# Kernel optimization log

Hardware: AMD Instinct MI355X
Metric: run time of the kernel (lower is better)

## Reference

```python
import jax, jax.numpy as jnp
import numpy as np

N_NODES = 100000
N_EDGES = 3200000
ENTITY_DIM = 128
LAYER_DIMS = [128, 64, 32]


def setup_inputs() -> dict:
    key = jax.random.key(0)
    ks = jax.random.split(key, 20)
    inp = {
        "x": jax.random.normal(ks[0], (N_NODES, ENTITY_DIM), dtype=jnp.float32) * 0.1,
        "src_idx": jax.random.randint(ks[1], (N_EDGES,), 0, N_NODES, dtype=jnp.int32),
        "dst_idx": jax.random.randint(ks[2], (N_EDGES,), 0, N_NODES, dtype=jnp.int32),
        "edge_attn": jax.random.uniform(ks[3], (N_EDGES,), dtype=jnp.float32),
    }
    in_dim = ENTITY_DIM
    ki = 4
    for li, out_dim in enumerate(LAYER_DIMS):
        scale = jnp.sqrt(2.0 / (in_dim + out_dim)).astype(jnp.float32)
        inp[f"W1_{li}"] = jax.random.normal(ks[ki], (in_dim, out_dim), dtype=jnp.float32) * scale
        inp[f"b1_{li}"] = jnp.zeros((out_dim,), dtype=jnp.float32)
        inp[f"W2_{li}"] = jax.random.normal(ks[ki + 1], (in_dim, out_dim), dtype=jnp.float32) * scale
        inp[f"b2_{li}"] = jnp.zeros((out_dim,), dtype=jnp.float32)
        ki += 2
        in_dim = out_dim
    return inp


def _kgat_layer(x, src_idx, dst_idx, a, W1, b1, W2, b2):
    # edge-weighted sparse aggregation: h_n[v] = sum_{(u->v)} a_e * x[u]
    msgs = x[src_idx] * a[:, None]                       # [E, D] gather + scale
    h_n = jax.ops.segment_sum(msgs, dst_idx, num_segments=x.shape[0])  # [N, D]
    # bi-interaction fuse
    out = jax.nn.leaky_relu((x + h_n) @ W1 + b1) + jax.nn.leaky_relu((x * h_n) @ W2 + b2)
    return out


def reference(x, src_idx, dst_idx, edge_attn,
              W1_0, b1_0, W2_0, b2_0,
              W1_1, b1_1, W2_1, b2_1,
              W1_2, b1_2, W2_2, b2_2):
    params = [(W1_0, b1_0, W2_0, b2_0), (W1_1, b1_1, W2_1, b2_1), (W1_2, b1_2, W2_2, b2_2)]
    embs = [x]
    h = x
    for (W1, b1, W2, b2) in params:
        h = _kgat_layer(h, src_idx, dst_idx, edge_attn, W1, b1, W2, b2)
        embs.append(h)
    return jnp.concatenate(embs, axis=1)  # [N, 128+128+64+32]
```

## Files before the change

kernel.cpp:

```cpp
#include <hip/hip_runtime.h>
#include <hip/hip_bf16.h>

#define LRELU_SLOPE 0.01f

typedef __attribute__((ext_vector_type(8))) short short8;
typedef __attribute__((ext_vector_type(4))) float f32x4;

__device__ __forceinline__ unsigned int f2bf_rne(float f) {
    unsigned int u = __float_as_uint(f);
    u += 0x7FFFu + ((u >> 16) & 1u);
    return u >> 16;
}
__device__ __forceinline__ float bf_lo(unsigned int u) { return __uint_as_float(u << 16); }
__device__ __forceinline__ float bf_hi(unsigned int u) { return __uint_as_float(u & 0xFFFF0000u); }

__global__ void bucket_count_kernel(const int* __restrict__ dst,
                                    int* __restrict__ bucket_total, int E, int NB) {
    __shared__ int cnt[512];
    const int t = threadIdx.x;
    const int tile0 = blockIdx.x * 8192;
    for (int i = t; i < 512; i += 256) cnt[i] = 0;
    __syncthreads();
#pragma unroll
    for (int j = 0; j < 32; ++j) {
        int e = tile0 + j * 256 + t;
        if (e < E) atomicAdd(&cnt[dst[e] >> 8], 1);
    }
    __syncthreads();
    for (int i = t; i < NB; i += 256) {
        int c = cnt[i];
        if (c) atomicAdd(&bucket_total[i], c);
    }
}

__global__ void bucket_scan_kernel(const int* __restrict__ bucket_total,
                                   int* __restrict__ bucket_base,
                                   int* __restrict__ row_ptr, int NB, int n) {
    __shared__ int s[512];
    const int t = threadIdx.x;
    int c = (t < NB) ? bucket_total[t] : 0;
    s[t] = c;
    __syncthreads();
    for (int off = 1; off < 512; off <<= 1) {
        int v = (t >= off) ? s[t - off] : 0;
        __syncthreads();
        s[t] += v;
        __syncthreads();
    }
    if (t < NB) bucket_base[t] = s[t] - c;
    if (t == 511) {
        bucket_base[NB] = s[511];
        row_ptr[n] = s[511];
    }
}

__global__ void bucket_scatter_kernel(const int* __restrict__ dst,
                                      const int* __restrict__ src,
                                      const float* __restrict__ attn,
                                      const int* __restrict__ bucket_base,
                                      int* __restrict__ bucket_fill,
                                      int2* __restrict__ bsa,
                                      int E, int NB) {
    __shared__ int cnt[512];
    __shared__ int basef[512];
    const int t = threadIdx.x;
    const int tile0 = blockIdx.x * 4096;
    for (int i = t; i < 512; i += 256) cnt[i] = 0;
    __syncthreads();
    int d[16], lr[16];
#pragma unroll
    for (int j = 0; j < 16; ++j) {
        int e = tile0 + j * 256 + t;
        if (e < E) {
            d[j] = dst[e];
            lr[j] = atomicAdd(&cnt[d[j] >> 8], 1);
        }
    }
    __syncthreads();
    for (int i = t; i < NB; i += 256) {
        int c = cnt[i];
        int r = c ? atomicAdd(&bucket_fill[i], c) : 0;
        basef[i] = bucket_base[i] + r;
    }
    __syncthreads();
#pragma unroll
    for (int j = 0; j < 16; ++j) {
        int e = tile0 + j * 256 + t;
        if (e < E) {
            int pos = basef[d[j] >> 8] + lr[j];
            unsigned int px = ((unsigned int)src[e] << 8) | (unsigned int)(d[j] & 255);
            bsa[pos] = make_int2((int)px, __float_as_int(attn[e]));
        }
    }
}

__global__ void bucket_build_kernel(const int* __restrict__ bucket_base,
                                    const int2* __restrict__ bsa,
                                    int* __restrict__ row_ptr, int2* __restrict__ csr_edge,
                                    int n) {
    __shared__ int cnt[256];
    __shared__ int pre[256];
    __shared__ int cur[256];
    const int t = threadIdx.x;
    const int k = blockIdx.x;
    const int base = bucket_base[k];
    const int M = bucket_base[k + 1] - base;
    const int node0 = k << 8;
    if (t < 256) cnt[t] = 0;
    __syncthreads();
    for (int i = t; i < M; i += 1024)
        atomicAdd(&cnt[(unsigned int)bsa[base + i].x & 255u], 1);
    __syncthreads();
    if (t < 256) pre[t] = cnt[t];
    __syncthreads();
    for (int off = 1; off < 256; off <<= 1) {
        int v = (t < 256 && t >= off) ? pre[t - off] : 0;
        __syncthreads();
        if (t < 256) pre[t] += v;
        __syncthreads();
    }
    if (t < 256) {
        pre[t] -= cnt[t];
        cur[t] = pre[t];
        int dnode = node0 + t;
        if (dnode < n) row_ptr[dnode] = base + pre[t];
    }
    __syncthreads();
    for (int i = t; i < M; i += 1024) {
        int2 sa = bsa[base + i];
        unsigned int px = (unsigned int)sa.x;
        int local = (int)(px & 255u);
        int p = base + atomicAdd(&cur[local], 1);
        csr_edge[p] = make_int2((int)(px >> 8), sa.y);
    }
}

__global__ void count_rank_kernel(const int* __restrict__ dst, int* __restrict__ counts,
                                  int* __restrict__ rank, int E) {
    const int base = blockIdx.x * (blockDim.x * 4) + threadIdx.x;
#pragma unroll
    for (int j = 0; j < 4; ++j) {
        int e = base + j * 256;
        if (e < E) rank[e] = atomicAdd(&counts[dst[e]], 1);
    }
}

__global__ void count_kernel(const int* __restrict__ dst, int* __restrict__ counts, int E) {
    int e = blockIdx.x * blockDim.x + threadIdx.x;
    if (e < E) atomicAdd(&counts[dst[e]], 1);
}

__global__ void scan_blocks_kernel(int* __restrict__ counts, int* __restrict__ row_ptr,
                                   int* __restrict__ partials, int n) {
    __shared__ int s[1024];
    const int t = threadIdx.x;
    const int i = blockIdx.x * 1024 + t;
    int c = (i < n) ? counts[i] : 0;
    s[t] = c;
    __syncthreads();
    for (int off = 1; off < 1024; off <<= 1) {
        int v = (t >= off) ? s[t - off] : 0;
        __syncthreads();
        s[t] += v;
        __syncthreads();
    }
    if (i < n) {
        row_ptr[i] = s[t] - c;
        counts[i] = 0;
    }
    if (t == 1023) partials[blockIdx.x] = s[1023];
}

__global__ void scan_partials_kernel(int* __restrict__ partials, int* __restrict__ row_ptr,
                                     int G, int n) {
    __shared__ int s[1024];
    const int t = threadIdx.x;
    int c = (t < G) ? partials[t] : 0;
    s[t] = c;
    __syncthreads();
    for (int off = 1; off < 1024; off <<= 1) {
        int v = (t >= off) ? s[t - off] : 0;
        __syncthreads();
        s[t] += v;
        __syncthreads();
    }
    if (t < G) partials[t] = s[t] - c;
    if (t == 1023) row_ptr[n] = s[1023];
}

__global__ void scan_add_kernel(int* __restrict__ row_ptr, const int* __restrict__ partials, int n) {
    int i = blockIdx.x * blockDim.x + threadIdx.x;
    if (i < n) row_ptr[i] += partials[i >> 10];
}

__global__ void fill_rank_kernel(const int* __restrict__ src, const int* __restrict__ dst,
                                 const float* __restrict__ attn,
                                 const int* __restrict__ row_ptr, const int* __restrict__ rank,
                                 int2* __restrict__ csr_edge, int E) {
    const int base = blockIdx.x * (blockDim.x * 4) + threadIdx.x;
    int  e[4], d[4], r[4], s[4];
    float a[4];
    bool ok[4];
#pragma unroll
    for (int j = 0; j < 4; ++j) {
        e[j] = base + j * 256;
        ok[j] = e[j] < E;
        int idx = ok[j] ? e[j] : 0;
        d[j] = dst[idx];
        r[j] = rank[idx];
        s[j] = src[idx];
        a[j] = attn[idx];
    }
    int p[4];
#pragma unroll
    for (int j = 0; j < 4; ++j) p[j] = row_ptr[d[j]] + r[j];
#pragma unroll
    for (int j = 0; j < 4; ++j)
        if (ok[j]) csr_edge[p[j]] = make_int2(s[j], __float_as_int(a[j]));
}

__global__ void fill_kernel(const int* __restrict__ src, const int* __restrict__ dst,
                            const float* __restrict__ attn,
                            const int* __restrict__ row_ptr, int* __restrict__ counts,
                            int2* __restrict__ csr_edge, int E) {
    int e = blockIdx.x * blockDim.x + threadIdx.x;
    if (e < E) {
        int d = dst[e];
        int pos = row_ptr[d] + atomicAdd(&counts[d], 1);
        csr_edge[pos] = make_int2(src[e], __float_as_int(attn[e]));
    }
}

__global__ void copy_cvt_kernel(const float4* __restrict__ x, float4* __restrict__ out,
                                uint2* __restrict__ xb, int n4) {
    int i = blockIdx.x * blockDim.x + threadIdx.x;
    if (i < n4) {
        float4 v = x[i];
        int nd = i >> 5;
        int c = i & 31;
        out[(long)nd * 88 + c] = v;
        xb[i] = make_uint2(f2bf_rne(v.x) | (f2bf_rne(v.y) << 16),
                           f2bf_rne(v.z) | (f2bf_rne(v.w) << 16));
    }
}

__global__ void copy_x_kernel(const float4* __restrict__ x, float4* __restrict__ out, int n4) {
    int i = blockIdx.x * blockDim.x + threadIdx.x;
    if (i < n4) {
        int v = i >> 5;
        int c = i & 31;
        out[(long)v * 88 + c] = x[i];
    }
}

__global__ void wtrans_kernel(const float* __restrict__ W, unsigned short* __restrict__ WT,
                              int in_dim, int out_dim) {
    int idx = blockIdx.x * blockDim.x + threadIdx.x;
    if (idx < in_dim * out_dim) {
        int o = idx / in_dim;
        int k = idx - o * in_dim;
        WT[idx] = (unsigned short)f2bf_rne(W[(long)k * out_dim + o]);
    }
}

__global__ void agg128_bf_kernel(const unsigned int* __restrict__ xb,
                                 const int* __restrict__ row_ptr,
                                 const int2* __restrict__ csr_edge,
                                 float* __restrict__ hagg, int n_nodes) {
    const int lane = threadIdx.x & 63;
    const int wid = (blockIdx.x * blockDim.x + threadIdx.x) >> 6;
    if (wid >= n_nodes) return;
    const int e0 = __builtin_amdgcn_readfirstlane(row_ptr[wid]);
    const int e1 = __builtin_amdgcn_readfirstlane(row_ptr[wid + 1]);
    float2 accA = {0.f, 0.f}, accB = {0.f, 0.f};
    int e = e0;
    for (; e + 4 <= e1; e += 4) {
        int2 p0 = csr_edge[e + 0];
        int2 p1 = csr_edge[e + 1];
        int2 p2 = csr_edge[e + 2];
        int2 p3 = csr_edge[e + 3];
        unsigned int u0 = xb[(long)p0.x * 64 + lane];
        unsigned int u1 = xb[(long)p1.x * 64 + lane];
        unsigned int u2 = xb[(long)p2.x * 64 + lane];
        unsigned int u3 = xb[(long)p3.x * 64 + lane];
        float a0 = __int_as_float(p0.y), a1 = __int_as_float(p1.y);
        float a2 = __int_as_float(p2.y), a3 = __int_as_float(p3.y);
        accA.x = fmaf(a0, bf_lo(u0), accA.x); accA.y = fmaf(a0, bf_hi(u0), accA.y);
        accB.x = fmaf(a1, bf_lo(u1), accB.x); accB.y = fmaf(a1, bf_hi(u1), accB.y);
        accA.x = fmaf(a2, bf_lo(u2), accA.x); accA.y = fmaf(a2, bf_hi(u2), accA.y);
        accB.x = fmaf(a3, bf_lo(u3), accB.x); accB.y = fmaf(a3, bf_hi(u3), accB.y);
    }
    for (; e < e1; ++e) {
        int2 p = csr_edge[e];
        unsigned int u = xb[(long)p.x * 64 + lane];
        float a = __int_as_float(p.y);
        accA.x = fmaf(a, bf_lo(u), accA.x); accA.y = fmaf(a, bf_hi(u), accA.y);
    }
    accA.x += accB.x; accA.y += accB.y;
    reinterpret_cast<float2*>(hagg + (long)wid * 128)[lane] = accA;
}

__global__ void agg64_bf_kernel(const unsigned int* __restrict__ xb,
                                const int* __restrict__ row_ptr,
                                const int2* __restrict__ csr_edge,
                                float* __restrict__ hagg, int n_nodes) {
    const int lane = threadIdx.x & 63;
    const int half = lane >> 5;
    const int l = lane & 31;
    const int wid = (blockIdx.x * blockDim.x + threadIdx.x) >> 6;
    if (wid >= n_nodes) return;
    const int e0 = __builtin_amdgcn_readfirstlane(row_ptr[wid]);
    const int e1 = __builtin_amdgcn_readfirstlane(row_ptr[wid + 1]);
    float2 accA = {0.f, 0.f}, accB = {0.f, 0.f};
    int e = e0;
    for (; e + 4 <= e1; e += 4) {
        int2 pA = csr_edge[e + half];
        int2 pB = csr_edge[e + 2 + half];
        unsigned int uA = xb[(long)pA.x * 32 + l];
        unsigned int uB = xb[(long)pB.x * 32 + l];
        float aA = __int_as_float(pA.y), aB = __int_as_float(pB.y);
        accA.x = fmaf(aA, bf_lo(uA), accA.x); accA.y = fmaf(aA, bf_hi(uA), accA.y);
        accB.x = fmaf(aB, bf_lo(uB), accB.x); accB.y = fmaf(aB, bf_hi(uB), accB.y);
    }
    if (e + 2 <= e1) {
        int2 p = csr_edge[e + half];
        unsigned int u = xb[(long)p.x * 32 + l];
        float a = __int_as_float(p.y);
        accA.x = fmaf(a, bf_lo(u), accA.x); accA.y = fmaf(a, bf_hi(u), accA.y);
        e += 2;
    }
    if (e < e1 && half == 0) {
        int2 p = csr_edge[e];
        unsigned int u = xb[(long)p.x * 32 + l];
        float a = __int_as_float(p.y);
        accA.x = fmaf(a, bf_lo(u), accA.x); accA.y = fmaf(a, bf_hi(u), accA.y);
    }
    accA.x += accB.x; accA.y += accB.y;
    accA.x += __shfl_xor(accA.x, 32);
    accA.y += __shfl_xor(accA.y, 32);
    if (half == 0) {
        reinterpret_cast<float2*>(hagg + (long)wid * 64)[l] = accA;
    }
}

template <int D>
__global__ void agg_f32_kernel(const float* __restrict__ xin, long xstride,
                               const int* __restrict__ row_ptr,
                               const int2* __restrict__ csr_edge,
                               float* __restrict__ hagg, int n_nodes) {
    const int lane = threadIdx.x & 63;
    const int wid = (blockIdx.x * blockDim.x + threadIdx.x) >> 6;
    if (wid >= n_nodes) return;
    const int e0 = row_ptr[wid], e1 = row_ptr[wid + 1];
    if (D == 128) {
        float2 accA = {0.f, 0.f}, accB = {0.f, 0.f};
        int e = e0;
        for (; e + 4 <= e1; e += 4) {
            int2 p0 = csr_edge[e + 0];
            int2 p1 = csr_edge[e + 1];
            int2 p2 = csr_edge[e + 2];
            int2 p3 = csr_edge[e + 3];
            float2 x0 = reinterpret_cast<const float2*>(xin + (long)p0.x * xstride)[lane];
            float2 x1 = reinterpret_cast<const float2*>(xin + (long)p1.x * xstride)[lane];
            float2 x2 = reinterpret_cast<const float2*>(xin + (long)p2.x * xstride)[lane];
            float2 x3 = reinterpret_cast<const float2*>(xin + (long)p3.x * xstride)[lane];
            float a0 = __int_as_float(p0.y), a1 = __int_as_float(p1.y);
            float a2 = __int_as_float(p2.y), a3 = __int_as_float(p3.y);
            accA.x = fmaf(a0, x0.x, accA.x); accA.y = fmaf(a0, x0.y, accA.y);
            accB.x = fmaf(a1, x1.x, accB.x); accB.y = fmaf(a1, x1.y, accB.y);
            accA.x = fmaf(a2, x2.x, accA.x); accA.y = fmaf(a2, x2.y, accA.y);
            accB.x = fmaf(a3, x3.x, accB.x); accB.y = fmaf(a3, x3.y, accB.y);
        }
        for (; e < e1; ++e) {
            int2 p = csr_edge[e];
            float2 xv = reinterpret_cast<const float2*>(xin + (long)p.x * xstride)[lane];
            float a = __int_as_float(p.y);
            accA.x = fmaf(a, xv.x, accA.x); accA.y = fmaf(a, xv.y, accA.y);
        }
        accA.x += accB.x; accA.y += accB.y;
        reinterpret_cast<float2*>(hagg + (long)wid * 128)[lane] = accA;
    } else {
        float accA = 0.f, accB = 0.f;
        int e = e0;
        for (; e + 4 <= e1; e += 4) {
            int2 p0 = csr_edge[e + 0];
            int2 p1 = csr_edge[e + 1];
            int2 p2 = csr_edge[e + 2];
            int2 p3 = csr_edge[e + 3];
            float x0 = xin[(long)p0.x * xstride + lane];
            float x1 = xin[(long)p1.x * xstride + lane];
            float x2 = xin[(long)p2.x * xstride + lane];
            float x3 = xin[(long)p3.x * xstride + lane];
            accA = fmaf(__int_as_float(p0.y), x0, accA);
            accB = fmaf(__int_as_float(p1.y), x1, accB);
            accA = fmaf(__int_as_float(p2.y), x2, accA);
            accB = fmaf(__int_as_float(p3.y), x3, accB);
        }
        for (; e < e1; ++e) {
            int2 p = csr_edge[e];
            accA = fmaf(__int_as_float(p.y), xin[(long)p.x * xstride + lane], accA);
        }
        hagg[(long)wid * 64 + lane] = accA + accB;
    }
}

template <int IN, int OUT>
__global__ __launch_bounds__(256) void mlp_mfma_kernel(
    const float* __restrict__ xin, long xstride,
    const float* __restrict__ hagg,
    const unsigned short* __restrict__ W1T, const float* __restrict__ b1,
    const unsigned short* __restrict__ W2T, const float* __restrict__ b2,
    float* __restrict__ out, long ostride,
    unsigned short* __restrict__ xb_next, int n_nodes)
{
    constexpr int BM  = 64;
    constexpr int NCH = IN / 8;
    constexpr int KK  = IN / 32;
    constexpr int NT  = OUT / 16;

    __shared__ uint4 xp_s[BM * NCH];
    __shared__ uint4 xm_s[BM * NCH];

    const int t = threadIdx.x;
    const int node0 = blockIdx.x * BM;

    for (int idx = t; idx < BM * NCH; idx += 256) {
        int n = idx / NCH;
        int c = idx - n * NCH;
        int v = node0 + n;
        int k = c * 8;
        float4 xa = {0.f,0.f,0.f,0.f}, xc = {0.f,0.f,0.f,0.f};
        float4 ha = {0.f,0.f,0.f,0.f}, hc = {0.f,0.f,0.f,0.f};
        if (v < n_nodes) {
            const float* xr = xin + (long)v * xstride + k;
            const float* hr = hagg + (long)v * IN + k;
            xa = *reinterpret_cast<const float4*>(xr);
            xc = *reinterpret_cast<const float4*>(xr + 4);
            ha = *reinterpret_cast<const float4*>(hr);
            hc = *reinterpret_cast<const float4*>(hr + 4);
        }
        uint4 up, um;
        up.x = f2bf_rne(xa.x + ha.x) | (f2bf_rne(xa.y + ha.y) << 16);
        up.y = f2bf_rne(xa.z + ha.z) | (f2bf_rne(xa.w + ha.w) << 16);
        up.z = f2bf_rne(xc.x + hc.x) | (f2bf_rne(xc.y + hc.y) << 16);
        up.w = f2bf_rne(xc.z + hc.z) | (f2bf_rne(xc.w + hc.w) << 16);
        um.x = f2bf_rne(xa.x * ha.x) | (f2bf_rne(xa.y * ha.y) << 16);
        um.y = f2bf_rne(xa.z * ha.z) | (f2bf_rne(xa.w * ha.w) << 16);
        um.z = f2bf_rne(xc.x * hc.x) | (f2bf_rne(xc.y * hc.y) << 16);
        um.w = f2bf_rne(xc.z * hc.z) | (f2bf_rne(xc.w * hc.w) << 16);
        int sc = c ^ (n & 7);
        xp_s[n * NCH + sc] = up;
        xm_s[n * NCH + sc] = um;
    }
    __syncthreads();

    const int lane = t & 63;
    const int wv   = t >> 6;
    const int arow = lane & 15;
    const int kgrp = lane >> 4;
    const int lrow = wv * 16 + arow;

    short8 ap[KK], am[KK];
#pragma unroll
    for (int kk = 0; kk < KK; ++kk) {
        int c  = kk * 4 + kgrp;
        int sc = c ^ (lrow & 7);
        ap[kk] = *reinterpret_cast<const short8*>(&xp_s[lrow * NCH + sc]);
        am[kk] = *reinterpret_cast<const short8*>(&xm_s[lrow * NCH + sc]);
    }

    f32x4 acc1[NT], acc2[NT];
#pragma unroll
    for (int nt = 0; nt < NT; ++nt) {
        acc1[nt] = (f32x4){0.f, 0.f, 0.f, 0.f};
        acc2[nt] = (f32x4){0.f, 0.f, 0.f, 0.f};
    }

#pragma unroll
    for (int nt = 0; nt < NT; ++nt) {
        const long nb = (long)(nt * 16 + arow) * IN + kgrp * 8;
#pragma unroll
        for (int kk = 0; kk < KK; ++kk) {
            short8 bw1 = *reinterpret_cast<const short8*>(W1T + nb + kk * 32);
            acc1[nt] = __builtin_amdgcn_mfma_f32_16x16x32_bf16(ap[kk], bw1, acc1[nt], 0, 0, 0);
            short8 bw2 = *reinterpret_cast<const short8*>(W2T + nb + kk * 32);
            acc2[nt] = __builtin_amdgcn_mfma_f32_16x16x32_bf16(am[kk], bw2, acc2[nt], 0, 0, 0);
        }
    }

    const int mbase = node0 + wv * 16 + kgrp * 4;
#pragma unroll
    for (int nt = 0; nt < NT; ++nt) {
        int n = nt * 16 + arow;
        float bb1 = b1[n], bb2 = b2[n];
#pragma unroll
        for (int j = 0; j < 4; ++j) {
            int v = mbase + j;
            if (v < n_nodes) {
                float r1 = acc1[nt][j] + bb1;
                float r2 = acc2[nt][j] + bb2;
                r1 = r1 >= 0.f ? r1 : LRELU_SLOPE * r1;
                r2 = r2 >= 0.f ? r2 : LRELU_SLOPE * r2;
                float r = r1 + r2;
                out[(long)v * ostride + n] = r;
                if (xb_next) xb_next[(long)v * OUT + n] = (unsigned short)f2bf_rne(r);
            }
        }
    }
}

template <int IN, int OUT, int NT>
__global__ void mlp_kernel(const float* __restrict__ xin, long xstride,
                           const float* __restrict__ hagg,
                           const float* __restrict__ W1, const float* __restrict__ b1,
                           const float* __restrict__ W2, const float* __restrict__ b2,
                           float* __restrict__ out, long ostride,
                           unsigned short* __restrict__ xb_next, int n_nodes) {
    constexpr int SLOTS = 256 / OUT;
    constexpr int NPB = SLOTS * NT;
    __shared__ float s_xp[NPB][IN + 4];
    __shared__ float s_xm[NPB][IN + 4];
    const int t = threadIdx.x;
    const int o = t % OUT;
    const int slot = t / OUT;
    const int node0 = blockIdx.x * NPB;

    for (int idx = t; idx < NPB * (IN / 4); idx += 256) {
        int n = idx / (IN / 4), c = idx % (IN / 4);
        int k = c * 4;
        int v = node0 + n;
        float4 xv = {0.f, 0.f, 0.f, 0.f}, hv = {0.f, 0.f, 0.f, 0.f};
        if (v < n_nodes) {
            xv = *reinterpret_cast<const float4*>(xin + (long)v * xstride + k);
            hv = *reinterpret_cast<const float4*>(hagg + (long)v * IN + k);
        }
        *reinterpret_cast<float4*>(&s_xp[n][k]) =
            make_float4(xv.x + hv.x, xv.y + hv.y, xv.z + hv.z, xv.w + hv.w);
        *reinterpret_cast<float4*>(&s_xm[n][k]) =
            make_float4(xv.x * hv.x, xv.y * hv.y, xv.z * hv.z, xv.w * hv.w);
    }
    __syncthreads();

    float acc1[NT], acc2[NT];
#pragma unroll
    for (int j = 0; j < NT; ++j) { acc1[j] = 0.f; acc2[j] = 0.f; }

    for (int k = 0; k < IN; k += 4) {
        float w10 = W1[(k + 0) * OUT + o], w11 = W1[(k + 1) * OUT + o];
        float w12 = W1[(k + 2) * OUT + o], w13 = W1[(k + 3) * OUT + o];
        float w20 = W2[(k + 0) * OUT + o], w21 = W2[(k + 1) * OUT + o];
        float w22 = W2[(k + 2) * OUT + o], w23 = W2[(k + 3) * OUT + o];
#pragma unroll
        for (int j = 0; j < NT; ++j) {
            int n = slot * NT + j;
            float4 xp = *reinterpret_cast<const float4*>(&s_xp[n][k]);
            float4 xm = *reinterpret_cast<const float4*>(&s_xm[n][k]);
            acc1[j] = fmaf(xp.x, w10, acc1[j]); acc1[j] = fmaf(xp.y, w11, acc1[j]);
            acc1[j] = fmaf(xp.z, w12, acc1[j]); acc1[j] = fmaf(xp.w, w13, acc1[j]);
            acc2[j] = fmaf(xm.x, w20, acc2[j]); acc2[j] = fmaf(xm.y, w21, acc2[j]);
            acc2[j] = fmaf(xm.z, w22, acc2[j]); acc2[j] = fmaf(xm.w, w23, acc2[j]);
        }
    }

    const float bb1 = b1[o], bb2 = b2[o];
#pragma unroll
    for (int j = 0; j < NT; ++j) {
        int v = node0 + slot * NT + j;
        if (v < n_nodes) {
            float r1 = acc1[j] + bb1;
            float r2 = acc2[j] + bb2;
            r1 = r1 >= 0.f ? r1 : LRELU_SLOPE * r1;
            r2 = r2 >= 0.f ? r2 : LRELU_SLOPE * r2;
            float r = r1 + r2;
            out[(long)v * ostride + o] = r;
            if (xb_next) xb_next[(long)v * OUT + o] = (unsigned short)f2bf_rne(r);
        }
    }
}

extern "C" void kernel_launch(void* const* d_in, const int* in_sizes, int n_in,
                              void* d_out, int out_size, void* d_ws, size_t ws_size,
                              hipStream_t stream) {
    const float* x    = (const float*)d_in[0];
    const int*   src  = (const int*)d_in[1];
    const int*   dst  = (const int*)d_in[2];
    const float* attn = (const float*)d_in[3];
    const float* W1_0 = (const float*)d_in[4];
    const float* b1_0 = (const float*)d_in[5];
    const float* W2_0 = (const float*)d_in[6];
    const float* b2_0 = (const float*)d_in[7];
    const float* W1_1 = (const float*)d_in[8];
    const float* b1_1 = (const float*)d_in[9];
    const float* W2_1 = (const float*)d_in[10];
    const float* b2_1 = (const float*)d_in[11];
    const float* W1_2 = (const float*)d_in[12];
    const float* b1_2 = (const float*)d_in[13];
    const float* W2_2 = (const float*)d_in[14];
    const float* b2_2 = (const float*)d_in[15];
    float* out = (float*)d_out;

    const int N = in_sizes[0] / 128;
    const int E = in_sizes[1];

    char* w = (char*)d_ws;
    size_t off = 0;
    auto alloc = [&](size_t bytes) -> void* {
        void* p = w + off;
        off += (bytes + 511) & ~(size_t)511;
        return p;
    };
    int*          counts   = (int*)alloc((size_t)N * 4);
    int*          row_ptr  = (int*)alloc((size_t)(N + 1) * 4);
    int*          partials = (int*)alloc((size_t)1024 * 4);
    int2*         csr_edge = (int2*)alloc((size_t)E * 8);
    float*        h_agg    = (float*)alloc((size_t)N * 128 * 4);
    unsigned int* xb       = (unsigned int*)alloc((size_t)N * 128 * 2);
    unsigned short* w1t0   = (unsigned short*)alloc((size_t)128 * 128 * 2);
    unsigned short* w2t0   = (unsigned short*)alloc((size_t)128 * 128 * 2);
    unsigned short* w1t1   = (unsigned short*)alloc((size_t)64 * 128 * 2);
    unsigned short* w2t1   = (unsigned short*)alloc((size_t)64 * 128 * 2);
    unsigned short* w1t2   = (unsigned short*)alloc((size_t)32 * 64 * 2);
    unsigned short* w2t2   = (unsigned short*)alloc((size_t)32 * 64 * 2);
    const bool use_bf16 = (off <= ws_size);

    const int NB = (N + 255) >> 8;
    int* bucket_mem  = (int*)alloc((size_t)2 * NB * 4);
    int* bucket_base = (int*)alloc((size_t)(NB + 1) * 4);
    const size_t off_fast = off;

    int2* bsa = (int2*)h_agg;
    const bool use_fast = use_bf16 && (off_fast <= ws_size) && (NB <= 512) &&
                          (N <= (1 << 23)) &&
                          ((size_t)E * 8 <= (size_t)N * 512);

    int* rank = (int*)alloc((size_t)E * 4);
    const bool use_rank = (off <= ws_size);

    const int G = (N + 1023) / 1024;

    if (use_fast) {
        int* bucket_total = bucket_mem;
        int* bucket_fill  = bucket_mem + NB;
        hipMemsetAsync(bucket_mem, 0, (size_t)2 * NB * 4, stream);
        bucket_count_kernel<<<(E + 8191) / 8192, 256, 0, stream>>>(dst, bucket_total, E, NB);
        bucket_scan_kernel<<<1, 512, 0, stream>>>(bucket_total, bucket_base, row_ptr, NB, N);
        bucket_scatter_kernel<<<(E + 4095) / 4096, 256, 0, stream>>>(
            dst, src, attn, bucket_base, bucket_fill, bsa, E, NB);
        bucket_build_kernel<<<NB, 1024, 0, stream>>>(bucket_base, bsa,
                                                     row_ptr, csr_edge, N);
    } else {
        hipMemsetAsync(counts, 0, (size_t)N * 4, stream);
        if (use_rank) {
            count_rank_kernel<<<(E + 1023) / 1024, 256, 0, stream>>>(dst, counts, rank, E);
        } else {
            count_kernel<<<(E + 255) / 256, 256, 0, stream>>>(dst, counts, E);
        }
        scan_blocks_kernel<<<G, 1024, 0, stream>>>(counts, row_ptr, partials, N);
        scan_partials_kernel<<<1, 1024, 0, stream>>>(partials, row_ptr, G, N);
        scan_add_kernel<<<(N + 255) / 256, 256, 0, stream>>>(row_ptr, partials, N);
        if (use_rank) {
            fill_rank_kernel<<<(E + 1023) / 1024, 256, 0, stream>>>(src, dst, attn, row_ptr,
                                                                    rank, csr_edge, E);
        } else {
            fill_kernel<<<(E + 255) / 256, 256, 0, stream>>>(src, dst, attn, row_ptr, counts,
                                                             csr_edge, E);
        }
    }

    if (use_bf16) {
        copy_cvt_kernel<<<(N * 32 + 255) / 256, 256, 0, stream>>>(
            (const float4*)x, (float4*)out, (uint2*)xb, N * 32);

        wtrans_kernel<<<(128 * 128 + 255) / 256, 256, 0, stream>>>(W1_0, w1t0, 128, 128);
        wtrans_kernel<<<(128 * 128 + 255) / 256, 256, 0, stream>>>(W2_0, w2t0, 128, 128);
        wtrans_kernel<<<(128 * 64 + 255) / 256, 256, 0, stream>>>(W1_1, w1t1, 128, 64);
        wtrans_kernel<<<(128 * 64 + 255) / 256, 256, 0, stream>>>(W2_1, w2t1, 128, 64);
        wtrans_kernel<<<(64 * 32 + 255) / 256, 256, 0, stream>>>(W1_2, w1t2, 64, 32);
        wtrans_kernel<<<(64 * 32 + 255) / 256, 256, 0, stream>>>(W2_2, w2t2, 64, 32);

        agg128_bf_kernel<<<(N + 3) / 4, 256, 0, stream>>>(xb, row_ptr, csr_edge, h_agg, N);
        mlp_mfma_kernel<128, 128><<<(N + 63) / 64, 256, 0, stream>>>(
            x, 128, h_agg, w1t0, b1_0, w2t0, b2_0,
            out + 128, 352, (unsigned short*)xb, N);
        agg128_bf_kernel<<<(N + 3) / 4, 256, 0, stream>>>(xb, row_ptr, csr_edge, h_agg, N);
        mlp_mfma_kernel<128, 64><<<(N + 63) / 64, 256, 0, stream>>>(
            out + 128, 352, h_agg, w1t1, b1_1, w2t1, b2_1,
            out + 256, 352, (unsigned short*)xb, N);
        agg64_bf_kernel<<<(N + 3) / 4, 256, 0, stream>>>(xb, row_ptr, csr_edge, h_agg, N);
        mlp_mfma_kernel<64, 32><<<(N + 63) / 64, 256, 0, stream>>>(
            out + 256, 352, h_agg, w1t2, b1_2, w2t2, b2_2,
            out + 320, 352, (unsigned short*)nullptr, N);
    } else {
        copy_x_kernel<<<(N * 32 + 255) / 256, 256, 0, stream>>>((const float4*)x, (float4*)out, N * 32);
        agg_f32_kernel<128><<<(N + 3) / 4, 256, 0, stream>>>(x, 128, row_ptr, csr_edge, h_agg, N);
        mlp_kernel<128, 128, 4><<<(N + 7) / 8, 256, 0, stream>>>(x, 128, h_agg,
                                                                 W1_0, b1_0, W2_0, b2_0,
                                                                 out + 128, 352,
                                                                 (unsigned short*)nullptr, N);
        agg_f32_kernel<128><<<(N + 3) / 4, 256, 0, stream>>>(out + 128, 352, row_ptr, csr_edge, h_agg, N);
        mlp_kernel<128, 64, 4><<<(N + 15) / 16, 256, 0, stream>>>(out + 128, 352, h_agg,
                                                                  W1_1, b1_1, W2_1, b2_1,
                                                                  out + 256, 352,
                                                                  (unsigned short*)nullptr, N);
        agg_f32_kernel<64><<<(N + 3) / 4, 256, 0, stream>>>(out + 256, 352, row_ptr, csr_edge, h_agg, N);
        mlp_kernel<64, 32, 4><<<(N + 31) / 32, 256, 0, stream>>>(out + 256, 352, h_agg,
                                                                 W1_2, b1_2, W2_2, b2_2,
                                                                 out + 320, 352,
                                                                 (unsigned short*)nullptr, N);
    }
}
```

Baseline: 841.5 us.

## Pack CSR edges into 32-bit words and keep aggregates and MLP inputs in bf16

Each CSR edge becomes one 32-bit word holding a 17-bit source index and 15-bit quantized attention, which halves edge-list traffic in every aggregation pass. The aggregation kernels now write bf16 outputs instead of fp32, and the MLP kernels read bf16 x and h, so the ping-pong bf16 buffers replace the fp32 reads. The 128-wide aggregation is unrolled to 8 edges, and the six weight-transpose launches are merged into one. In exchange, attention is quantized to 15 bits and the hidden state is kept in bf16, which adds precision error, and the fast path is limited to at most 2^17 nodes.

```diff
diff --git a/kernel.cpp b/kernel.cpp
--- a/kernel.cpp
+++ b/kernel.cpp
@@ -13,6 +13,12 @@
 }
 __device__ __forceinline__ float bf_lo(unsigned int u) { return __uint_as_float(u << 16); }
 __device__ __forceinline__ float bf_hi(unsigned int u) { return __uint_as_float(u & 0xFFFF0000u); }
+
+__device__ __forceinline__ unsigned int pack_edge(int src, float a) {
+    int q = (int)(a * 32767.0f + 0.5f);
+    q = q < 0 ? 0 : (q > 32767 ? 32767 : q);
+    return ((unsigned int)src << 15) | (unsigned int)q;
+}
 
 __global__ void bucket_count_kernel(const int* __restrict__ dst,
                                     int* __restrict__ bucket_total, int E, int NB) {
@@ -96,7 +102,8 @@
 
 __global__ void bucket_build_kernel(const int* __restrict__ bucket_base,
                                     const int2* __restrict__ bsa,
-                                    int* __restrict__ row_ptr, int2* __restrict__ csr_edge,
+                                    int* __restrict__ row_ptr,
+                                    unsigned int* __restrict__ csr_pk,
                                     int n) {
     __shared__ int cnt[256];
     __shared__ int pre[256];
@@ -130,8 +137,9 @@
         int2 sa = bsa[base + i];
         unsigned int px = (unsigned int)sa.x;
         int local = (int)(px & 255u);
+        int srcv  = (int)(px >> 8);
         int p = base + atomicAdd(&cur[local], 1);
-        csr_edge[p] = make_int2((int)(px >> 8), sa.y);
+        csr_pk[p] = pack_edge(srcv, __int_as_float(sa.y));
     }
 }
 
@@ -196,7 +204,7 @@
 __global__ void fill_rank_kernel(const int* __restrict__ src, const int* __restrict__ dst,
                                  const float* __restrict__ attn,
                                  const int* __restrict__ row_ptr, const int* __restrict__ rank,
-                                 int2* __restrict__ csr_edge, int E) {
+                                 unsigned int* __restrict__ csr_pk, int E) {
     const int base = blockIdx.x * (blockDim.x * 4) + threadIdx.x;
     int  e[4], d[4], r[4], s[4];
     float a[4];
@@ -216,7 +224,7 @@
     for (int j = 0; j < 4; ++j) p[j] = row_ptr[d[j]] + r[j];
 #pragma unroll
     for (int j = 0; j < 4; ++j)
-        if (ok[j]) csr_edge[p[j]] = make_int2(s[j], __float_as_int(a[j]));
+        if (ok[j]) csr_pk[p[j]] = pack_edge(s[j], a[j]);
 }
 
 __global__ void fill_kernel(const int* __restrict__ src, const int* __restrict__ dst,
@@ -253,20 +261,30 @@
     }
 }
 
-__global__ void wtrans_kernel(const float* __restrict__ W, unsigned short* __restrict__ WT,
-                              int in_dim, int out_dim) {
-    int idx = blockIdx.x * blockDim.x + threadIdx.x;
-    if (idx < in_dim * out_dim) {
-        int o = idx / in_dim;
-        int k = idx - o * in_dim;
-        WT[idx] = (unsigned short)f2bf_rne(W[(long)k * out_dim + o]);
-    }
+__global__ void wtrans_all_kernel(const float* __restrict__ W1_0, const float* __restrict__ W2_0,
+                                  const float* __restrict__ W1_1, const float* __restrict__ W2_1,
+                                  const float* __restrict__ W1_2, const float* __restrict__ W2_2,
+                                  unsigned short* __restrict__ t10, unsigned short* __restrict__ t20,
+                                  unsigned short* __restrict__ t11, unsigned short* __restrict__ t21,
+                                  unsigned short* __restrict__ t12, unsigned short* __restrict__ t22) {
+    int i = blockIdx.x * blockDim.x + threadIdx.x;
+    const float* W; unsigned short* T; int in_d, out_d, base;
+    if      (i < 16384) { W = W1_0; T = t10; in_d = 128; out_d = 128; base = 0; }
+    else if (i < 32768) { W = W2_0; T = t20; in_d = 128; out_d = 128; base = 16384; }
+    else if (i < 40960) { W = W1_1; T = t11; in_d = 128; out_d = 64;  base = 32768; }
+    else if (i < 49152) { W = W2_1; T = t21; in_d = 128; out_d = 64;  base = 40960; }
+    else if (i < 51200) { W = W1_2; T = t12; in_d = 64;  out_d = 32;  base = 49152; }
+    else if (i < 53248) { W = W2_2; T = t22; in_d = 64;  out_d = 32;  base = 51200; }
+    else return;
+    int idx = i - base;
+    int o = idx / in_d, k = idx - o * in_d;
+    T[idx] = (unsigned short)f2bf_rne(W[(long)k * out_d + o]);
 }
 
 __global__ void agg128_bf_kernel(const unsigned int* __restrict__ xb,
                                  const int* __restrict__ row_ptr,
-                                 const int2* __restrict__ csr_edge,
-                                 float* __restrict__ hagg, int n_nodes) {
+                                 const unsigned int* __restrict__ csr,
+                                 unsigned int* __restrict__ hb, int n_nodes) {
     const int lane = threadIdx.x & 63;
     const int wid = (blockIdx.x * blockDim.x + threadIdx.x) >> 6;
     if (wid >= n_nodes) return;
@@ -274,36 +292,35 @@
     const int e1 = __builtin_amdgcn_readfirstlane(row_ptr[wid + 1]);
     float2 accA = {0.f, 0.f}, accB = {0.f, 0.f};
     int e = e0;
-    for (; e + 4 <= e1; e += 4) {
-        int2 p0 = csr_edge[e + 0];
-        int2 p1 = csr_edge[e + 1];
-        int2 p2 = csr_edge[e + 2];
-        int2 p3 = csr_edge[e + 3];
-        unsigned int u0 = xb[(long)p0.x * 64 + lane];
-        unsigned int u1 = xb[(long)p1.x * 64 + lane];
-        unsigned int u2 = xb[(long)p2.x * 64 + lane];
-        unsigned int u3 = xb[(long)p3.x * 64 + lane];
-        float a0 = __int_as_float(p0.y), a1 = __int_as_float(p1.y);
-        float a2 = __int_as_float(p2.y), a3 = __int_as_float(p3.y);
-        accA.x = fmaf(a0, bf_lo(u0), accA.x); accA.y = fmaf(a0, bf_hi(u0), accA.y);
-        accB.x = fmaf(a1, bf_lo(u1), accB.x); accB.y = fmaf(a1, bf_hi(u1), accB.y);
-        accA.x = fmaf(a2, bf_lo(u2), accA.x); accA.y = fmaf(a2, bf_hi(u2), accA.y);
-        accB.x = fmaf(a3, bf_lo(u3), accB.x); accB.y = fmaf(a3, bf_hi(u3), accB.y);
+    for (; e + 8 <= e1; e += 8) {
+        unsigned int px[8], u[8];
+#pragma unroll
+        for (int j = 0; j < 8; ++j) px[j] = csr[e + j];
+#pragma unroll
+        for (int j = 0; j < 8; ++j) u[j] = xb[(long)(px[j] >> 15) * 64 + lane];
+#pragma unroll
+        for (int j = 0; j < 8; ++j) {
+            float q = (float)(px[j] & 32767u);
+            if (j & 1) { accB.x = fmaf(q, bf_lo(u[j]), accB.x); accB.y = fmaf(q, bf_hi(u[j]), accB.y); }
+            else       { accA.x = fmaf(q, bf_lo(u[j]), accA.x); accA.y = fmaf(q, bf_hi(u[j]), accA.y); }
+        }
     }
     for (; e < e1; ++e) {
-        int2 p = csr_edge[e];
-        unsigned int u = xb[(long)p.x * 64 + lane];
-        float a = __int_as_float(p.y);
-        accA.x = fmaf(a, bf_lo(u), accA.x); accA.y = fmaf(a, bf_hi(u), accA.y);
-    }
-    accA.x += accB.x; accA.y += accB.y;
-    reinterpret_cast<float2*>(hagg + (long)wid * 128)[lane] = accA;
+        unsigned int px = csr[e];
+        unsigned int u = xb[(long)(px >> 15) * 64 + lane];
+        float q = (float)(px & 32767u);
+        accA.x = fmaf(q, bf_lo(u), accA.x); accA.y = fmaf(q, bf_hi(u), accA.y);
+    }
+    const float s = 1.0f / 32767.0f;
+    float hx = (accA.x + accB.x) * s;
+    float hy = (accA.y + accB.y) * s;
+    hb[(long)wid * 64 + lane] = f2bf_rne(hx) | (f2bf_rne(hy) << 16);
 }
 
 __global__ void agg64_bf_kernel(const unsigned int* __restrict__ xb,
                                 const int* __restrict__ row_ptr,
-                                const int2* __restrict__ csr_edge,
-                                float* __restrict__ hagg, int n_nodes) {
+                                const unsigned int* __restrict__ csr,
+                                unsigned int* __restrict__ hb, int n_nodes) {
     const int lane = threadIdx.x & 63;
     const int half = lane >> 5;
     const int l = lane & 31;
@@ -314,32 +331,33 @@
     float2 accA = {0.f, 0.f}, accB = {0.f, 0.f};
     int e = e0;
     for (; e + 4 <= e1; e += 4) {
-        int2 pA = csr_edge[e + half];
-        int2 pB = csr_edge[e + 2 + half];
-        unsigned int uA = xb[(long)pA.x * 32 + l];
-        unsigned int uB = xb[(long)pB.x * 32 + l];
-        float aA = __int_as_float(pA.y), aB = __int_as_float(pB.y);
-        accA.x = fmaf(aA, bf_lo(uA), accA.x); accA.y = fmaf(aA, bf_hi(uA), accA.y);
-        accB.x = fmaf(aB, bf_lo(uB), accB.x); accB.y = fmaf(aB, bf_hi(uB), accB.y);
+        unsigned int pA = csr[e + half];
+        unsigned int pB = csr[e + 2 + half];
+        unsigned int uA = xb[(long)(pA >> 15) * 32 + l];
+        unsigned int uB = xb[(long)(pB >> 15) * 32 + l];
+        float qA = (float)(pA & 32767u), qB = (float)(pB & 32767u);
+        accA.x = fmaf(qA, bf_lo(uA), accA.x); accA.y = fmaf(qA, bf_hi(uA), accA.y);
+        accB.x = fmaf(qB, bf_lo(uB), accB.x); accB.y = fmaf(qB, bf_hi(uB), accB.y);
     }
     if (e + 2 <= e1) {
-        int2 p = csr_edge[e + half];
-        unsigned int u = xb[(long)p.x * 32 + l];
-        float a = __int_as_float(p.y);
-        accA.x = fmaf(a, bf_lo(u), accA.x); accA.y = fmaf(a, bf_hi(u), accA.y);
+        unsigned int p = csr[e + half];
+        unsigned int u = xb[(long)(p >> 15) * 32 + l];
+        float q = (float)(p & 32767u);
+        accA.x = fmaf(q, bf_lo(u), accA.x); accA.y = fmaf(q, bf_hi(u), accA.y);
         e += 2;
     }
     if (e < e1 && half == 0) {
-        int2 p = csr_edge[e];
-        unsigned int u = xb[(long)p.x * 32 + l];
-        float a = __int_as_float(p.y);
-        accA.x = fmaf(a, bf_lo(u), accA.x); accA.y = fmaf(a, bf_hi(u), accA.y);
+        unsigned int p = csr[e];
+        unsigned int u = xb[(long)(p >> 15) * 32 + l];
+        float q = (float)(p & 32767u);
+        accA.x = fmaf(q, bf_lo(u), accA.x); accA.y = fmaf(q, bf_hi(u), accA.y);
     }
     accA.x += accB.x; accA.y += accB.y;
     accA.x += __shfl_xor(accA.x, 32);
     accA.y += __shfl_xor(accA.y, 32);
     if (half == 0) {
-        reinterpret_cast<float2*>(hagg + (long)wid * 64)[l] = accA;
+        const float s = 1.0f / 32767.0f;
+        hb[(long)wid * 32 + l] = f2bf_rne(accA.x * s) | (f2bf_rne(accA.y * s) << 16);
     }
 }
 
@@ -355,21 +373,14 @@
     if (D == 128) {
         float2 accA = {0.f, 0.f}, accB = {0.f, 0.f};
         int e = e0;
-        for (; e + 4 <= e1; e += 4) {
+        for (; e + 2 <= e1; e += 2) {
             int2 p0 = csr_edge[e + 0];
             int2 p1 = csr_edge[e + 1];
-            int2 p2 = csr_edge[e + 2];
-            int2 p3 = csr_edge[e + 3];
             float2 x0 = reinterpret_cast<const float2*>(xin + (long)p0.x * xstride)[lane];
             float2 x1 = reinterpret_cast<const float2*>(xin + (long)p1.x * xstride)[lane];
-            float2 x2 = reinterpret_cast<const float2*>(xin + (long)p2.x * xstride)[lane];
-            float2 x3 = reinterpret_cast<const float2*>(xin + (long)p3.x * xstride)[lane];
             float a0 = __int_as_float(p0.y), a1 = __int_as_float(p1.y);
-            float a2 = __int_as_float(p2.y), a3 = __int_as_float(p3.y);
             accA.x = fmaf(a0, x0.x, accA.x); accA.y = fmaf(a0, x0.y, accA.y);
             accB.x = fmaf(a1, x1.x, accB.x); accB.y = fmaf(a1, x1.y, accB.y);
-            accA.x = fmaf(a2, x2.x, accA.x); accA.y = fmaf(a2, x2.y, accA.y);
-            accB.x = fmaf(a3, x3.x, accB.x); accB.y = fmaf(a3, x3.y, accB.y);
         }
         for (; e < e1; ++e) {
             int2 p = csr_edge[e];
@@ -380,34 +391,19 @@
         accA.x += accB.x; accA.y += accB.y;
         reinterpret_cast<float2*>(hagg + (long)wid * 128)[lane] = accA;
     } else {
-        float accA = 0.f, accB = 0.f;
-        int e = e0;
-        for (; e + 4 <= e1; e += 4) {
-            int2 p0 = csr_edge[e + 0];
-            int2 p1 = csr_edge[e + 1];
-            int2 p2 = csr_edge[e + 2];
-            int2 p3 = csr_edge[e + 3];
-            float x0 = xin[(long)p0.x * xstride + lane];
-            float x1 = xin[(long)p1.x * xstride + lane];
-            float x2 = xin[(long)p2.x * xstride + lane];
-            float x3 = xin[(long)p3.x * xstride + lane];
-            accA = fmaf(__int_as_float(p0.y), x0, accA);
-            accB = fmaf(__int_as_float(p1.y), x1, accB);
-            accA = fmaf(__int_as_float(p2.y), x2, accA);
-            accB = fmaf(__int_as_float(p3.y), x3, accB);
-        }
-        for (; e < e1; ++e) {
+        float accA = 0.f;
+        for (int e = e0; e < e1; ++e) {
             int2 p = csr_edge[e];
             accA = fmaf(__int_as_float(p.y), xin[(long)p.x * xstride + lane], accA);
         }
-        hagg[(long)wid * 64 + lane] = accA + accB;
+        hagg[(long)wid * 64 + lane] = accA;
     }
 }
 
 template <int IN, int OUT>
 __global__ __launch_bounds__(256) void mlp_mfma_kernel(
-    const float* __restrict__ xin, long xstride,
-    const float* __restrict__ hagg,
+    const unsigned int* __restrict__ xin_bf,
+    const unsigned int* __restrict__ hagg_bf,
     const unsigned short* __restrict__ W1T, const float* __restrict__ b1,
     const unsigned short* __restrict__ W2T, const float* __restrict__ b2,
     float* __restrict__ out, long ostride,
@@ -417,6 +413,7 @@
     constexpr int NCH = IN / 8;
     constexpr int KK  = IN / 32;
     constexpr int NT  = OUT / 16;
+    constexpr int RU  = IN / 2;
 
     __shared__ uint4 xp_s[BM * NCH];
     __shared__ uint4 xm_s[BM * NCH];
@@ -428,26 +425,32 @@
         int n = idx / NCH;
         int c = idx - n * NCH;
         int v = node0 + n;
-        int k = c * 8;
-        float4 xa = {0.f,0.f,0.f,0.f}, xc = {0.f,0.f,0.f,0.f};
-        float4 ha = {0.f,0.f,0.f,0.f}, hc = {0.f,0.f,0.f,0.f};
+        uint4 xv = {0u,0u,0u,0u}, hv = {0u,0u,0u,0u};
         if (v < n_nodes) {
-            const float* xr = xin + (long)v * xstride + k;
-            const float* hr = hagg + (long)v * IN + k;
-            xa = *reinterpret_cast<const float4*>(xr);
-            xc = *reinterpret_cast<const float4*>(xr + 4);
-            ha = *reinterpret_cast<const float4*>(hr);
-            hc = *reinterpret_cast<const float4*>(hr + 4);
+            xv = *reinterpret_cast<const uint4*>(xin_bf  + (long)v * RU + c * 4);
+            hv = *reinterpret_cast<const uint4*>(hagg_bf + (long)v * RU + c * 4);
         }
         uint4 up, um;
-        up.x = f2bf_rne(xa.x + ha.x) | (f2bf_rne(xa.y + ha.y) << 16);
-        up.y = f2bf_rne(xa.z + ha.z) | (f2bf_rne(xa.w + ha.w) << 16);
-        up.z = f2bf_rne(xc.x + hc.x) | (f2bf_rne(xc.y + hc.y) << 16);
-        up.w = f2bf_rne(xc.z + hc.z) | (f2bf_rne(xc.w + hc.w) << 16);
-        um.x = f2bf_rne(xa.x * ha.x) | (f2bf_rne(xa.y * ha.y) << 16);
-        um.y = f2bf_rne(xa.z * ha.z) | (f2bf_rne(xa.w * ha.w) << 16);
-        um.z = f2bf_rne(xc.x * hc.x) | (f2bf_rne(xc.y * hc.y) << 16);
-        um.w = f2bf_rne(xc.z * hc.z) | (f2bf_rne(xc.w * hc.w) << 16);
+        {
+            float xl = bf_lo(xv.x), xh = bf_hi(xv.x), hl = bf_lo(hv.x), hh = bf_hi(hv.x);
+            up.x = f2bf_rne(xl + hl) | (f2bf_rne(xh + hh) << 16);
+            um.x = f2bf_rne(xl * hl) | (f2bf_rne(xh * hh) << 16);
+        }
+        {
+            float xl = bf_lo(xv.y), xh = bf_hi(xv.y), hl = bf_lo(hv.y), hh = bf_hi(hv.y);
+            up.y = f2bf_rne(xl + hl) | (f2bf_rne(xh + hh) << 16);
+            um.y = f2bf_rne(xl * hl) | (f2bf_rne(xh * hh) << 16);
+        }
+        {
+            float xl = bf_lo(xv.z), xh = bf_hi(xv.z), hl = bf_lo(hv.z), hh = bf_hi(hv.z);
+            up.z = f2bf_rne(xl + hl) | (f2bf_rne(xh + hh) << 16);
+            um.z = f2bf_rne(xl * hl) | (f2bf_rne(xh * hh) << 16);
+        }
+        {
+            float xl = bf_lo(xv.w), xh = bf_hi(xv.w), hl = bf_lo(hv.w), hh = bf_hi(hv.w);
+            up.w = f2bf_rne(xl + hl) | (f2bf_rne(xh + hh) << 16);
+            um.w = f2bf_rne(xl * hl) | (f2bf_rne(xh * hh) << 16);
+        }
         int sc = c ^ (n & 7);
         xp_s[n * NCH + sc] = up;
         xm_s[n * NCH + sc] = um;
@@ -612,16 +615,17 @@
     int*          counts   = (int*)alloc((size_t)N * 4);
     int*          row_ptr  = (int*)alloc((size_t)(N + 1) * 4);
     int*          partials = (int*)alloc((size_t)1024 * 4);
-    int2*         csr_edge = (int2*)alloc((size_t)E * 8);
+    unsigned int* csr_pk   = (unsigned int*)alloc((size_t)E * 8);
     float*        h_agg    = (float*)alloc((size_t)N * 128 * 4);
-    unsigned int* xb       = (unsigned int*)alloc((size_t)N * 128 * 2);
+    unsigned int* xb_a     = (unsigned int*)alloc((size_t)N * 128 * 2);
+    unsigned int* xb_b     = (unsigned int*)alloc((size_t)N * 128 * 2);
     unsigned short* w1t0   = (unsigned short*)alloc((size_t)128 * 128 * 2);
     unsigned short* w2t0   = (unsigned short*)alloc((size_t)128 * 128 * 2);
     unsigned short* w1t1   = (unsigned short*)alloc((size_t)64 * 128 * 2);
     unsigned short* w2t1   = (unsigned short*)alloc((size_t)64 * 128 * 2);
     unsigned short* w1t2   = (unsigned short*)alloc((size_t)32 * 64 * 2);
     unsigned short* w2t2   = (unsigned short*)alloc((size_t)32 * 64 * 2);
-    const bool use_bf16 = (off <= ws_size);
+    const bool use_bf16 = (off <= ws_size) && (N <= (1 << 17));
 
     const int NB = (N + 255) >> 8;
     int* bucket_mem  = (int*)alloc((size_t)2 * NB * 4);
@@ -630,13 +634,13 @@
 
     int2* bsa = (int2*)h_agg;
     const bool use_fast = use_bf16 && (off_fast <= ws_size) && (NB <= 512) &&
-                          (N <= (1 << 23)) &&
                           ((size_t)E * 8 <= (size_t)N * 512);
 
     int* rank = (int*)alloc((size_t)E * 4);
-    const bool use_rank = (off <= ws_size);
+    const bool use_rank = use_bf16 && (off <= ws_size);
 
     const int G = (N + 1023) / 1024;
+    unsigned int* h_bf = (unsigned int*)h_agg;
 
     if (use_fast) {
         int* bucket_total = bucket_mem;
@@ -646,9 +650,8 @@
         bucket_scan_kernel<<<1, 512, 0, stream>>>(bucket_total, bucket_base, row_ptr, NB, N);
         bucket_scatter_kernel<<<(E + 4095) / 4096, 256, 0, stream>>>(
             dst, src, attn, bucket_base, bucket_fill, bsa, E, NB);
-        bucket_build_kernel<<<NB, 1024, 0, stream>>>(bucket_base, bsa,
-                                                     row_ptr, csr_edge, N);
-    } else {
+        bucket_build_kernel<<<NB, 1024, 0, stream>>>(bucket_base, bsa, row_ptr, csr_pk, N);
+    } else if (use_bf16) {
         hipMemsetAsync(counts, 0, (size_t)N * 4, stream);
         if (use_rank) {
             count_rank_kernel<<<(E + 1023) / 1024, 256, 0, stream>>>(dst, counts, rank, E);
@@ -660,49 +663,52 @@
         scan_add_kernel<<<(N + 255) / 256, 256, 0, stream>>>(row_ptr, partials, N);
         if (use_rank) {
             fill_rank_kernel<<<(E + 1023) / 1024, 256, 0, stream>>>(src, dst, attn, row_ptr,
-                                                                    rank, csr_edge, E);
+                                                                    rank, csr_pk, E);
         } else {
-            fill_kernel<<<(E + 255) / 256, 256, 0, stream>>>(src, dst, attn, row_ptr, counts,
-                                                             csr_edge, E);
-        }
+            fill_rank_kernel<<<(E + 1023) / 1024, 256, 0, stream>>>(src, dst, attn, row_ptr,
+                                                                    rank, csr_pk, E);
+        }
+    } else {
+        hipMemsetAsync(counts, 0, (size_t)N * 4, stream);
+        count_kernel<<<(E + 255) / 256, 256, 0, stream>>>(dst, counts, E);
+        scan_blocks_kernel<<<G, 1024, 0, stream>>>(counts, row_ptr, partials, N);
+        scan_partials_kernel<<<1, 1024, 0, stream>>>(partials, row_ptr, G, N);
+        scan_add_kernel<<<(N + 255) / 256, 256, 0, stream>>>(row_ptr, partials, N);
+        fill_kernel<<<(E + 255) / 256, 256, 0, stream>>>(src, dst, attn, row_ptr, counts,
+                                                         (int2*)csr_pk, E);
     }
 
     if (use_bf16) {
         copy_cvt_kernel<<<(N * 32 + 255) / 256, 256, 0, stream>>>(
-            (const float4*)x, (float4*)out, (uint2*)xb, N * 32);
-
-        wtrans_kernel<<<(128 * 128 + 255) / 256, 256, 0, stream>>>(W1_0, w1t0, 128, 128);
-        wtrans_kernel<<<(128 * 128 + 255) / 256, 256, 0, stream>>>(W2_0, w2t0, 128, 128);
-        wtrans_kernel<<<(128 * 64 + 255) / 256, 256, 0, stream>>>(W1_1, w1t1, 128, 64);
-        wtrans_kernel<<<(128 * 64 + 255) / 256, 256, 0, stream>>>(W2_1, w2t1, 128, 64);
-        wtrans_kernel<<<(64 * 32 + 255) / 256, 256, 0, stream>>>(W1_2, w1t2, 64, 32);
-        wtrans_kernel<<<(64 * 32 + 255) / 256, 256, 0, stream>>>(W2_2, w2t2, 64, 32);
-
-        agg128_bf_kernel<<<(N + 3) / 4, 256, 0, stream>>>(xb, row_ptr, csr_edge, h_agg, N);
+            (const float4*)x, (float4*)out, (uint2*)xb_a, N * 32);
+        wtrans_all_kernel<<<208, 256, 0, stream>>>(W1_0, W2_0, W1_1, W2_1, W1_2, W2_2,
+                                                   w1t0, w2t0, w1t1, w2t1, w1t2, w2t2);
+
+        agg128_bf_kernel<<<(N + 3) / 4, 256, 0, stream>>>(xb_a, row_ptr, csr_pk, h_bf, N);
         mlp_mfma_kernel<128, 128><<<(N + 63) / 64, 256, 0, stream>>>(
-            x, 128, h_agg, w1t0, b1_0, w2t0, b2_0,
-            out + 128, 352, (unsigned short*)xb, N);
-        agg128_bf_kernel<<<(N + 3) / 4, 256, 0, stream>>>(xb, row_ptr, csr_edge, h_agg, N);
+            xb_a, h_bf, w1t0, b1_0, w2t0, b2_0,
+            out + 128, 352, (unsigned short*)xb_b, N);
+        agg128_bf_kernel<<<(N + 3) / 4, 256, 0, stream>>>(xb_b, row_ptr, csr_pk, h_bf, N);
         mlp_mfma_kernel<128, 64><<<(N + 63) / 64, 256, 0, stream>>>(
-            out + 128, 352, h_agg, w1t1, b1_1, w2t1, b2_1,
-            out + 256, 352, (unsigned short*)xb, N);
-        agg64_bf_kernel<<<(N + 3) / 4, 256, 0, stream>>>(xb, row_ptr, csr_edge, h_agg, N);
+            xb_b, h_bf, w1t1, b1_1, w2t1, b2_1,
+            out + 256, 352, (unsigned short*)xb_a, N);
+        agg64_bf_kernel<<<(N + 3) / 4, 256, 0, stream>>>(xb_a, row_ptr, csr_pk, h_bf, N);
         mlp_mfma_kernel<64, 32><<<(N + 63) / 64, 256, 0, stream>>>(
-            out + 256, 352, h_agg, w1t2, b1_2, w2t2, b2_2,
+            xb_a, h_bf, w1t2, b1_2, w2t2, b2_2,
             out + 320, 352, (unsigned short*)nullptr, N);
     } else {
         copy_x_kernel<<<(N * 32 + 255) / 256, 256, 0, stream>>>((const float4*)x, (float4*)out, N * 32);
-        agg_f32_kernel<128><<<(N + 3) / 4, 256, 0, stream>>>(x, 128, row_ptr, csr_edge, h_agg, N);
+        agg_f32_kernel<128><<<(N + 3) / 4, 256, 0, stream>>>(x, 128, row_ptr, (const int2*)csr_pk, h_agg, N);
         mlp_kernel<128, 128, 4><<<(N + 7) / 8, 256, 0, stream>>>(x, 128, h_agg,
                                                                  W1_0, b1_0, W2_0, b2_0,
                                                                  out + 128, 352,
                                                                  (unsigned short*)nullptr, N);
-        agg_f32_kernel<128><<<(N + 3) / 4, 256, 0, stream>>>(out + 128, 352, row_ptr, csr_edge, h_agg, N);
+        agg_f32_kernel<128><<<(N + 3) / 4, 256, 0, stream>>>(out + 128, 352, row_ptr, (const int2*)csr_pk, h_agg, N);
         mlp_kernel<128, 64, 4><<<(N + 15) / 16, 256, 0, stream>>>(out + 128, 352, h_agg,
                                                                   W1_1, b1_1, W2_1, b2_1,
                                                                   out + 256, 352,
                                                                   (unsigned short*)nullptr, N);
-        agg_f32_kernel<64><<<(N + 3) / 4, 256, 0, stream>>>(out + 256, 352, row_ptr, csr_edge, h_agg, N);
+        agg_f32_kernel<64><<<(N + 3) / 4, 256, 0, stream>>>(out + 256, 352, row_ptr, (const int2*)csr_pk, h_agg, N);
         mlp_kernel<64, 32, 4><<<(N + 31) / 32, 256, 0, stream>>>(out + 256, 352, h_agg,
                                                                  W1_2, b1_2, W2_2, b2_2,
                                                                  out + 320, 352,
```

Result: faster. 802.4 us (-4.6%).
